# Kernel tuning notes

Measured on AMD Instinct MI355X. Metric: run time of the kernel, lower is better.

Reference implementation:

```python
import jax, jax.numpy as jnp
import numpy as np

B, T, D_IN, D_H = 32, 2048, 256, 256


def setup_inputs() -> dict:
    key = jax.random.key(0)
    k1, k2, k3 = jax.random.split(key, 3)
    s_in = 1.0 / np.sqrt(D_IN)
    s_h = 1.0 / np.sqrt(D_H)
    return {
        "x": jax.random.normal(k1, (B, T, D_IN), dtype=jnp.float32),
        "h": jnp.zeros((B, D_H), dtype=jnp.float32),
        "W_in": jax.random.normal(k2, (D_IN, D_H), dtype=jnp.float32) * s_in,
        "b_in": jnp.zeros((D_H,), dtype=jnp.float32),
        "W_h": jax.random.normal(k3, (D_H, D_H), dtype=jnp.float32) * s_h,
        "b_h": jnp.zeros((D_H,), dtype=jnp.float32),
    }


def reference(x, h, W_in, b_in, W_h, b_h):
    # x: [B, T, D_in] (batch_first). Precompute input projection for all t
    # (mathematically identical, avoids T tiny GEMMs on x).
    x_proj = jnp.einsum("btd,dh->bth", x, W_in) + b_in  # [B, T, H]
    x_proj_t = jnp.swapaxes(x_proj, 0, 1)  # time-major [T, B, H]

    def step(h_prev, xp_t):
        h_new = jax.nn.relu(xp_t + h_prev @ W_h + b_h)  # [B, H]
        return h_new, h_new

    _, hs = jax.lax.scan(step, h, x_proj_t)  # hs: [T, B, H]
    return jnp.swapaxes(hs, 0, 1)  # [B, T, H]
```

## Files before the change

kernel.cpp:

```cpp
#include <hip/hip_runtime.h>

#define T_LEN 2048
#define DH 256
#define NCHUNK (T_LEN / 16)

typedef short short8 __attribute__((ext_vector_type(8)));
typedef float f32x4 __attribute__((ext_vector_type(4)));

__device__ __forceinline__ unsigned short f2bf(float f) {
  unsigned u = __builtin_bit_cast(unsigned, f);
  u += 0x7fffu + ((u >> 16) & 1u);
  return (unsigned short)(u >> 16);
}

#define WG_BARRIER() do {                                   \
  __builtin_amdgcn_sched_barrier(0);                        \
  asm volatile("s_waitcnt lgkmcnt(0)" ::: "memory");        \
  __builtin_amdgcn_s_barrier();                             \
  __builtin_amdgcn_sched_barrier(0);                        \
} while (0)

__global__ __launch_bounds__(256, 1) void xproj_gemm(
    const float* __restrict__ x, const float* __restrict__ W_in,
    const float* __restrict__ b_in, const float* __restrict__ b_h,
    float* __restrict__ out) {
  const int tid  = threadIdx.x;
  const int lane = tid & 63;
  const int w    = tid >> 6;
  const int l15  = lane & 15;
  const int lg   = lane >> 4;
  const int koff = lg * 8;
  const int m0   = blockIdx.x * 128;

  short8 Bf[4][8];
#pragma unroll
  for (int n = 0; n < 4; ++n) {
    const int c = 64 * w + 16 * n + l15;
#pragma unroll
    for (int kk = 0; kk < 8; ++kk) {
      short8 bf;
#pragma unroll
      for (int j = 0; j < 8; ++j)
        bf[j] = (short)f2bf(W_in[(32 * kk + koff + j) * DH + c]);
      Bf[n][kk] = bf;
    }
  }
  float bin[4];
#pragma unroll
  for (int n = 0; n < 4; ++n) {
    const int c = 64 * w + 16 * n + l15;
    bin[n] = b_in[c] + b_h[c];
  }

  for (int slab = 0; slab < 8; ++slab) {
    const float* xr = x + (size_t)(m0 + slab * 16 + l15) * DH;
    short8 A[8];
#pragma unroll
    for (int kk = 0; kk < 8; ++kk) {
      f32x4 v0 = *(const f32x4*)(xr + 32 * kk + koff);
      f32x4 v1 = *(const f32x4*)(xr + 32 * kk + koff + 4);
      short8 a;
      a[0] = f2bf(v0[0]); a[1] = f2bf(v0[1]); a[2] = f2bf(v0[2]); a[3] = f2bf(v0[3]);
      a[4] = f2bf(v1[0]); a[5] = f2bf(v1[1]); a[6] = f2bf(v1[2]); a[7] = f2bf(v1[3]);
      A[kk] = a;
    }
    f32x4 acc[4];
#pragma unroll
    for (int n = 0; n < 4; ++n) acc[n] = (f32x4){0.f, 0.f, 0.f, 0.f};
#pragma unroll
    for (int kk = 0; kk < 8; ++kk)
#pragma unroll
      for (int n = 0; n < 4; ++n)
        acc[n] = __builtin_amdgcn_mfma_f32_16x16x32_bf16(A[kk], Bf[n][kk], acc[n], 0, 0, 0);
#pragma unroll
    for (int n = 0; n < 4; ++n) {
      const int c = 64 * w + 16 * n + l15;
#pragma unroll
      for (int r = 0; r < 4; ++r)
        out[(size_t)(m0 + slab * 16 + lg * 4 + r) * DH + c] = acc[n][r] + bin[n];
    }
  }
}

__global__ __launch_bounds__(512, 2) void rnn_scan(
    const float* __restrict__ h0, const float* __restrict__ W_h,
    float* __restrict__ out) {
  __shared__ __align__(16) unsigned short hbuf[2][DH];
  __shared__ __align__(16) float xpb[2][16 * DH];
  __shared__ __align__(16) float xout[16 * DH];

  const int tid  = threadIdx.x;
  const int lane = tid & 63;
  const int w    = tid >> 6;
  const int l15  = lane & 15;
  const int lg   = lane >> 4;
  const int koff = lg * 8;
  const int b    = blockIdx.x;
  float* outb = out + (size_t)b * T_LEN * DH;

  f32x4 st[2];
#pragma unroll
  for (int i = 0; i < 2; ++i)
    st[i] = *(const f32x4*)(outb + i * 2048 + tid * 4);

  short8 Bf[2][8];
#pragma unroll
  for (int n = 0; n < 2; ++n) {
    const int c = 32 * w + 16 * n + l15;
#pragma unroll
    for (int kk = 0; kk < 8; ++kk) {
      short8 bf;
#pragma unroll
      for (int j = 0; j < 8; ++j)
        bf[j] = (short)f2bf(W_h[(32 * kk + koff + j) * DH + c]);
      Bf[n][kk] = bf;
    }
  }

  if (tid < DH) hbuf[0][tid] = f2bf(h0[b * DH + tid]);
#pragma unroll
  for (int i = 0; i < 2; ++i)
    *(f32x4*)(&xpb[0][i * 2048 + tid * 4]) = st[i];
#pragma unroll
  for (int i = 0; i < 2; ++i)
    st[i] = *(const f32x4*)(outb + 4096 + i * 2048 + tid * 4);
  __syncthreads();

  short8 A[8];
#pragma unroll
  for (int kk = 0; kk < 8; ++kk) A[kk] = (short8){0, 0, 0, 0, 0, 0, 0, 0};

  for (int t = 0; t < T_LEN; ++t) {
    const unsigned short* hb = &hbuf[t & 1][0];
    if (l15 == 0) {
#pragma unroll
      for (int kk = 0; kk < 8; ++kk)
        A[kk] = *(const short8*)(hb + 32 * kk + koff);
    }
    float xb[2];
    if (lane < 16) {
#pragma unroll
      for (int n = 0; n < 2; ++n)
        xb[n] = xpb[(t >> 4) & 1][(t & 15) * DH + 32 * w + 16 * n + lane];
    }

    f32x4 ac[2][2];
#pragma unroll
    for (int n = 0; n < 2; ++n) {
      ac[n][0] = (f32x4){0.f, 0.f, 0.f, 0.f};
      ac[n][1] = (f32x4){0.f, 0.f, 0.f, 0.f};
    }
#pragma unroll
    for (int kk = 0; kk < 4; ++kk)
#pragma unroll
      for (int n = 0; n < 2; ++n)
        ac[n][0] = __builtin_amdgcn_mfma_f32_16x16x32_bf16(A[kk], Bf[n][kk], ac[n][0], 0, 0, 0);
#pragma unroll
    for (int kk = 4; kk < 8; ++kk)
#pragma unroll
      for (int n = 0; n < 2; ++n)
        ac[n][1] = __builtin_amdgcn_mfma_f32_16x16x32_bf16(A[kk], Bf[n][kk], ac[n][1], 0, 0, 0);

    if (lane < 16) {
#pragma unroll
      for (int n = 0; n < 2; ++n) {
        const int c = 32 * w + 16 * n + lane;
        float v = ac[n][0][0] + ac[n][1][0] + xb[n];
        v = fmaxf(v, 0.0f);
        xout[(t & 15) * DH + c] = v;
        hbuf[(t + 1) & 1][c] = f2bf(v);
      }
    }

    if ((t & 15) == 15) {
      WG_BARRIER();
      const int cc = t >> 4;
      const int nc = cc + 1;
      if (nc < NCHUNK) {
#pragma unroll
        for (int i = 0; i < 2; ++i)
          *(f32x4*)(&xpb[nc & 1][i * 2048 + tid * 4]) = st[i];
        const int pc = nc + 1;
        if (pc < NCHUNK) {
#pragma unroll
          for (int i = 0; i < 2; ++i)
            st[i] = *(const f32x4*)(outb + (size_t)pc * 4096 + i * 2048 + tid * 4);
        }
      }
      f32x4 o[2];
#pragma unroll
      for (int i = 0; i < 2; ++i)
        o[i] = *(const f32x4*)(&xout[i * 2048 + tid * 4]);
#pragma unroll
      for (int i = 0; i < 2; ++i)
        *(f32x4*)(outb + (size_t)cc * 4096 + i * 2048 + tid * 4) = o[i];
      WG_BARRIER();
    } else {
      WG_BARRIER();
    }
  }
}

extern "C" void kernel_launch(void* const* d_in, const int* in_sizes, int n_in,
                              void* d_out, int out_size, void* d_ws, size_t ws_size,
                              hipStream_t stream) {
  const float* x    = (const float*)d_in[0];
  const float* h0   = (const float*)d_in[1];
  const float* W_in = (const float*)d_in[2];
  const float* b_in = (const float*)d_in[3];
  const float* W_h  = (const float*)d_in[4];
  const float* b_h  = (const float*)d_in[5];
  float* out = (float*)d_out;

  hipLaunchKernelGGL(xproj_gemm, dim3(512), dim3(256), 0, stream, x, W_in, b_in, b_h, out);
  hipLaunchKernelGGL(rnn_scan, dim3(32), dim3(512), 0, stream, h0, W_h, out);
}
```

Measured before the change: 910.2 us.

## Prefetch x-projection into registers and store RNN outputs directly to global

Replaces the LDS staging buffers for the input projection and the output with per-lane register arrays (two chunks of 16 steps, double-buffered) loaded straight from global memory, and writes each step's outputs directly to global instead of through LDS. This removes the extra chunk-boundary barrier and the bulk LDS copy work, and makes every step uniform. In exchange it raises register pressure with 64 extra floats per lane, makes the loads and stores narrow and scattered, and leaves the global-load latency hidden only by the prefetch distance. There is also a risk that outstanding global loads stall step barriers.

```diff
diff --git a/kernel.cpp b/kernel.cpp
--- a/kernel.cpp
+++ b/kernel.cpp
@@ -13,8 +13,7 @@
   return (unsigned short)(u >> 16);
 }
 
-#define WG_BARRIER() do {                                   \
-  __builtin_amdgcn_sched_barrier(0);                        \
+#define STEP_BARRIER() do {                                 \
   asm volatile("s_waitcnt lgkmcnt(0)" ::: "memory");        \
   __builtin_amdgcn_s_barrier();                             \
   __builtin_amdgcn_sched_barrier(0);                        \
@@ -85,9 +84,7 @@
 __global__ __launch_bounds__(512, 2) void rnn_scan(
     const float* __restrict__ h0, const float* __restrict__ W_h,
     float* __restrict__ out) {
-  __shared__ __align__(16) unsigned short hbuf[2][DH];
-  __shared__ __align__(16) float xpb[2][16 * DH];
-  __shared__ __align__(16) float xout[16 * DH];
+  __shared__ __align__(16) unsigned short hb[2][DH];
 
   const int tid  = threadIdx.x;
   const int lane = tid & 63;
@@ -98,10 +95,21 @@
   const int b    = blockIdx.x;
   float* outb = out + (size_t)b * T_LEN * DH;
 
-  f32x4 st[2];
+  float xbA[32], xbB[32];
+
+  auto ISSUE_XB = [&](int cc, float (&xb)[32]) {
+    if (cc < NCHUNK && lane < 16) {
+      const float* p = outb + (size_t)cc * 16 * DH + 32 * w + l15;
 #pragma unroll
-  for (int i = 0; i < 2; ++i)
-    st[i] = *(const f32x4*)(outb + i * 2048 + tid * 4);
+      for (int s = 0; s < 16; ++s) {
+        xb[2 * s]     = p[(size_t)s * DH];
+        xb[2 * s + 1] = p[(size_t)s * DH + 16];
+      }
+    }
+  };
+
+  ISSUE_XB(0, xbA);
+  ISSUE_XB(1, xbB);
 
   short8 Bf[2][8];
 #pragma unroll
@@ -117,87 +125,60 @@
     }
   }
 
-  if (tid < DH) hbuf[0][tid] = f2bf(h0[b * DH + tid]);
-#pragma unroll
-  for (int i = 0; i < 2; ++i)
-    *(f32x4*)(&xpb[0][i * 2048 + tid * 4]) = st[i];
-#pragma unroll
-  for (int i = 0; i < 2; ++i)
-    st[i] = *(const f32x4*)(outb + 4096 + i * 2048 + tid * 4);
+  if (tid < DH) hb[0][tid] = f2bf(h0[b * DH + tid]);
   __syncthreads();
 
   short8 A[8];
 #pragma unroll
   for (int kk = 0; kk < 8; ++kk) A[kk] = (short8){0, 0, 0, 0, 0, 0, 0, 0};
 
-  for (int t = 0; t < T_LEN; ++t) {
-    const unsigned short* hb = &hbuf[t & 1][0];
-    if (l15 == 0) {
+  auto CHUNK = [&](int cc, float (&xb)[32]) {
+    float* orow = outb + (size_t)cc * 16 * DH;
 #pragma unroll
-      for (int kk = 0; kk < 8; ++kk)
-        A[kk] = *(const short8*)(hb + 32 * kk + koff);
-    }
-    float xb[2];
-    if (lane < 16) {
+    for (int s = 0; s < 16; ++s) {
+      const unsigned short* hbR = hb[s & 1];
+      unsigned short* hbW = hb[(s + 1) & 1];
+      if (l15 == 0) {
 #pragma unroll
-      for (int n = 0; n < 2; ++n)
-        xb[n] = xpb[(t >> 4) & 1][(t & 15) * DH + 32 * w + 16 * n + lane];
-    }
+        for (int kk = 0; kk < 8; ++kk)
+          A[kk] = *(const short8*)(hbR + 32 * kk + koff);
+      }
 
-    f32x4 ac[2][2];
-#pragma unroll
-    for (int n = 0; n < 2; ++n) {
-      ac[n][0] = (f32x4){0.f, 0.f, 0.f, 0.f};
-      ac[n][1] = (f32x4){0.f, 0.f, 0.f, 0.f};
-    }
-#pragma unroll
-    for (int kk = 0; kk < 4; ++kk)
-#pragma unroll
-      for (int n = 0; n < 2; ++n)
-        ac[n][0] = __builtin_amdgcn_mfma_f32_16x16x32_bf16(A[kk], Bf[n][kk], ac[n][0], 0, 0, 0);
-#pragma unroll
-    for (int kk = 4; kk < 8; ++kk)
-#pragma unroll
-      for (int n = 0; n < 2; ++n)
-        ac[n][1] = __builtin_amdgcn_mfma_f32_16x16x32_bf16(A[kk], Bf[n][kk], ac[n][1], 0, 0, 0);
-
-    if (lane < 16) {
+      f32x4 ac[2][2];
 #pragma unroll
       for (int n = 0; n < 2; ++n) {
-        const int c = 32 * w + 16 * n + lane;
-        float v = ac[n][0][0] + ac[n][1][0] + xb[n];
-        v = fmaxf(v, 0.0f);
-        xout[(t & 15) * DH + c] = v;
-        hbuf[(t + 1) & 1][c] = f2bf(v);
+        ac[n][0] = (f32x4){0.f, 0.f, 0.f, 0.f};
+        ac[n][1] = (f32x4){0.f, 0.f, 0.f, 0.f};
       }
+#pragma unroll
+      for (int kk = 0; kk < 4; ++kk)
+#pragma unroll
+        for (int n = 0; n < 2; ++n)
+          ac[n][0] = __builtin_amdgcn_mfma_f32_16x16x32_bf16(A[kk], Bf[n][kk], ac[n][0], 0, 0, 0);
+#pragma unroll
+      for (int kk = 4; kk < 8; ++kk)
+#pragma unroll
+        for (int n = 0; n < 2; ++n)
+          ac[n][1] = __builtin_amdgcn_mfma_f32_16x16x32_bf16(A[kk], Bf[n][kk], ac[n][1], 0, 0, 0);
+
+      if (lane < 16) {
+        float v0 = (ac[0][0][0] + ac[0][1][0]) + xb[2 * s];
+        float v1 = (ac[1][0][0] + ac[1][1][0]) + xb[2 * s + 1];
+        v0 = fmaxf(v0, 0.0f);
+        v1 = fmaxf(v1, 0.0f);
+        hbW[32 * w + lane]      = f2bf(v0);
+        hbW[32 * w + 16 + lane] = f2bf(v1);
+        orow[(size_t)s * DH + 32 * w + lane]      = v0;
+        orow[(size_t)s * DH + 32 * w + 16 + lane] = v1;
+      }
+      STEP_BARRIER();
     }
+    ISSUE_XB(cc + 2, xb);
+  };
 
-    if ((t & 15) == 15) {
-      WG_BARRIER();
-      const int cc = t >> 4;
-      const int nc = cc + 1;
-      if (nc < NCHUNK) {
-#pragma unroll
-        for (int i = 0; i < 2; ++i)
-          *(f32x4*)(&xpb[nc & 1][i * 2048 + tid * 4]) = st[i];
-        const int pc = nc + 1;
-        if (pc < NCHUNK) {
-#pragma unroll
-          for (int i = 0; i < 2; ++i)
-            st[i] = *(const f32x4*)(outb + (size_t)pc * 4096 + i * 2048 + tid * 4);
-        }
-      }
-      f32x4 o[2];
-#pragma unroll
-      for (int i = 0; i < 2; ++i)
-        o[i] = *(const f32x4*)(&xout[i * 2048 + tid * 4]);
-#pragma unroll
-      for (int i = 0; i < 2; ++i)
-        *(f32x4*)(outb + (size_t)cc * 4096 + i * 2048 + tid * 4) = o[i];
-      WG_BARRIER();
-    } else {
-      WG_BARRIER();
-    }
+  for (int c2 = 0; c2 < NCHUNK; c2 += 2) {
+    CHUNK(c2, xbA);
+    CHUNK(c2 + 1, xbB);
   }
 }
 
```

Result: faster. 840.9 us (-7.6%).
